# Kernel tuning notes

Hardware: AMD Instinct MI355X
Metric: run time of the kernel (lower is better)

The kernel has to match this reference:

```python
import jax, jax.numpy as jnp
import numpy as np

B, N, IN_DIM, HID, OUT, E = 2, 50000, 64, 256, 128, 500000

def setup_inputs() -> dict:
    key = jax.random.key(0)
    ks = jax.random.split(key, 8)
    s = lambda fan_in: 1.0 / np.sqrt(fan_in)
    x = jax.random.normal(ks[0], (B, N, IN_DIM), dtype=jnp.float32)
    edges = jax.random.randint(ks[1], (E, 2), 0, N, dtype=jnp.int64)
    return {
        "x": x,
        "edges": edges,
        "ew1": jax.random.normal(ks[2], (2 * IN_DIM, HID), dtype=jnp.float32) * s(2 * IN_DIM),
        "eb1": jnp.zeros((HID,), jnp.float32),
        "ew2": jax.random.normal(ks[3], (HID, OUT), dtype=jnp.float32) * s(HID),
        "eb2": jnp.zeros((OUT,), jnp.float32),
        "nw1": jax.random.normal(ks[4], (IN_DIM, HID), dtype=jnp.float32) * s(IN_DIM),
        "nb1": jnp.zeros((HID,), jnp.float32),
        "nw2": jax.random.normal(ks[5], (HID, OUT), dtype=jnp.float32) * s(HID),
        "nb2": jnp.zeros((OUT,), jnp.float32),
        "dw": jax.random.normal(ks[6], (OUT, IN_DIM), dtype=jnp.float32) * s(OUT),
        "db": jnp.zeros((IN_DIM,), jnp.float32),
    }

def _mlp(z, w1, b1, w2, b2):
    return jax.nn.relu(z @ w1 + b1) @ w2 + b2

def reference(x, edges, ew1, eb1, ew2, eb2, nw1, nb1, nw2, nb2, dw, db):
    u, v = edges[:, 0], edges[:, 1]
    # node embedding: [B, N, OUT]
    h = _mlp(x, nw1, nb1, nw2, nb2)
    # per-edge MLP on concatenated endpoint features: [B, E, OUT]
    edge_input = jnp.concatenate([x[:, u], x[:, v]], axis=-1)  # [B, E, 2*IN]
    edge_emb = _mlp(edge_input, ew1, eb1, ew2, eb2)
    # scatter-add edge message to both endpoints
    messages = jnp.zeros_like(h).at[:, u].add(edge_emb).at[:, v].add(edge_emb)
    h = h + messages
    recon = h @ dw + db  # [B, N, IN]
    return recon
```

## Files before the change

kernel.cpp:

```cpp
#include <hip/hip_runtime.h>
#include <hip/hip_bf16.h>

#define BB   2
#define NN   50000
#define BN   100000
#define NE   500000
#define NSB  196

#define EPITCH 136
#define XPITCH 72
#define HPITCH 264
#define RPITCH 72

using u16 = unsigned short;
using u32 = unsigned int;
typedef __attribute__((ext_vector_type(8))) short short8;
typedef __attribute__((ext_vector_type(4))) short short4v;
typedef __attribute__((ext_vector_type(4))) float f32x4;

__device__ __forceinline__ u16 f2bf(float f) {
    union { float f; u32 u; } w; w.f = f;
    return (u16)((w.u + 0x7fffu + ((w.u >> 16) & 1u)) >> 16);
}

__global__ __launch_bounds__(256) void csr_zero(int* __restrict__ cursor) {
    int i = blockIdx.x * 256 + threadIdx.x;
    if (i < NN) cursor[i] = 0;
}

__global__ __launch_bounds__(256) void csr_hist(const int* __restrict__ edges,
                                                int* __restrict__ cursor) {
    int e = blockIdx.x * 256 + threadIdx.x;
    if (e < NE) {
        atomicAdd(&cursor[edges[2*e]], 1);
        atomicAdd(&cursor[edges[2*e+1]], 1);
    }
}

__global__ __launch_bounds__(256) void scan_pass1(const int* __restrict__ cursor,
                                                  int* __restrict__ bsum) {
    __shared__ int s[256];
    const int t = threadIdx.x;
    int i = blockIdx.x * 256 + t;
    s[t] = (i < NN) ? cursor[i] : 0;
    __syncthreads();
    for (int d = 128; d > 0; d >>= 1) {
        if (t < d) s[t] += s[t + d];
        __syncthreads();
    }
    if (t == 0) bsum[blockIdx.x] = s[0];
}

__global__ __launch_bounds__(256) void scan_pass2(const int* __restrict__ bsum,
                                                  int* __restrict__ boff) {
    __shared__ int s[256];
    const int t = threadIdx.x;
    s[t] = (t < NSB) ? bsum[t] : 0;
    __syncthreads();
    for (int d = 1; d < 256; d <<= 1) {
        int v = (t >= d) ? s[t - d] : 0;
        __syncthreads();
        s[t] += v;
        __syncthreads();
    }
    if (t <= NSB) boff[t] = (t == 0) ? 0 : s[t - 1];
}

__global__ __launch_bounds__(256) void scan_pass3(int* __restrict__ cursor,
                                                  const int* __restrict__ boff,
                                                  int* __restrict__ off) {
    __shared__ int s[256];
    const int t = threadIdx.x;
    int i = blockIdx.x * 256 + t;
    int v = (i < NN) ? cursor[i] : 0;
    s[t] = v;
    __syncthreads();
    for (int d = 1; d < 256; d <<= 1) {
        int p = (t >= d) ? s[t - d] : 0;
        __syncthreads();
        s[t] += p;
        __syncthreads();
    }
    int excl = boff[blockIdx.x] + s[t] - v;
    if (i < NN) { off[i] = excl; cursor[i] = excl; }
    if (i == NN - 1) off[NN] = excl + v;
}

__global__ __launch_bounds__(256) void csr_fill(const int* __restrict__ edges,
                                                int* __restrict__ cursor,
                                                int* __restrict__ pos) {
    int e = blockIdx.x * 256 + threadIdx.x;
    if (e < NE) {
        pos[2*e]     = atomicAdd(&cursor[edges[2*e]], 1);
        pos[2*e + 1] = atomicAdd(&cursor[edges[2*e+1]], 1);
    }
}

__global__ __launch_bounds__(256) void swizzle_w1(
    const float* __restrict__ ew1, const float* __restrict__ nw1,
    u16* __restrict__ frag)
{
    int idx = blockIdx.x * 256 + threadIdx.x;
    if (idx >= 49152) return;
    const float* src; int KB, local;
    if (idx < 32768) { local = idx;         src = ew1; KB = 4; }
    else             { local = idx - 32768; src = nw1; KB = 2; }
    int j = local & 7, l = (local >> 3) & 63, rest = local >> 9;
    int kblk = rest % KB, ntile = rest / KB;
    int n = ntile * 16 + (l & 15);
    int k = kblk * 32 + ((l >> 4) << 3) + j;
    frag[idx] = f2bf(src[k * 256 + n]);
}

__global__ __launch_bounds__(256) void fuse_w2(
    const float* __restrict__ ew2, const float* __restrict__ nw2,
    const float* __restrict__ dw, u16* __restrict__ frag)
{
    int idx = blockIdx.x * 256 + threadIdx.x;
    if (idx >= 32768) return;
    const float* src = (idx < 16384) ? ew2 : nw2;
    int local = idx & 16383;
    int j = local & 7, l = (local >> 3) & 63, rest = local >> 9;
    int kblk = rest & 7, ntile = rest >> 3;
    int n = ntile * 16 + (l & 15);
    int k = kblk * 32 + ((l >> 4) << 3) + j;
    float s = 0.f;
    for (int jj = 0; jj < 128; ++jj) s = fmaf(src[k * 128 + jj], dw[jj * 64 + n], s);
    frag[49152 + idx] = f2bf(s);
}

__global__ __launch_bounds__(64) void fuse_bias(
    const float* __restrict__ eb2, const float* __restrict__ nb2,
    const float* __restrict__ dw, const float* __restrict__ db,
    float* __restrict__ bias2)
{
    int d = threadIdx.x;
    float se = 0.f, sn = 0.f;
    for (int j = 0; j < 128; ++j) {
        float w = dw[j * 64 + d];
        se = fmaf(eb2[j], w, se);
        sn = fmaf(nb2[j], w, sn);
    }
    bias2[d] = se;
    bias2[64 + d] = sn + db[d];
}

__global__ __launch_bounds__(256) void x_to_bf16(const float* __restrict__ x,
                                                 u16* __restrict__ xbf)
{
    int i = blockIdx.x * 256 + threadIdx.x;
    if (i >= BN * 16) return;
    float4 g = ((const float4*)x)[i];
    short4v s;
    s.x = (short)f2bf(g.x); s.y = (short)f2bf(g.y);
    s.z = (short)f2bf(g.z); s.w = (short)f2bf(g.w);
    *(short4v*)(xbf + (size_t)i * 4) = s;
}

__global__ __launch_bounds__(256) void node_mlp_kernel(
    const u16* __restrict__ xbf, const float* __restrict__ nb1,
    const float* __restrict__ bias2, const u16* __restrict__ frag,
    float* __restrict__ out)
{
    __shared__ u16 xs[64 * XPITCH];
    __shared__ u16 hid[64 * HPITCH];
    const int t = threadIdx.x;
    const int wave = t >> 6, l = t & 63, lane15 = l & 15, quad = l >> 4;
    const int r0 = blockIdx.x * 64;
    const int valid = min(64, BN - r0);

    #pragma unroll
    for (int it = 0; it < 2; ++it) {
        int i = t + it * 256;
        int m = i >> 3, c8 = i & 7;
        int row = min(r0 + m, BN - 1);
        uint4 q = ((const uint4*)xbf)[(size_t)row * 8 + c8];
        *(uint4*)(xs + m * XPITCH + c8 * 8) = q;
    }
    __syncthreads();

    {
        f32x4 acc[4][4];
        #pragma unroll
        for (int i = 0; i < 4; ++i)
            #pragma unroll
            for (int mt = 0; mt < 4; ++mt) acc[i][mt] = f32x4{0.f,0.f,0.f,0.f};
        const u16* w1 = frag + 32768;
        #pragma unroll
        for (int kblk = 0; kblk < 2; ++kblk) {
            short8 bf[4], af[4];
            #pragma unroll
            for (int mt = 0; mt < 4; ++mt)
                bf[mt] = *(const short8*)(xs + (mt*16 + lane15) * XPITCH + kblk*32 + quad*8);
            #pragma unroll
            for (int i = 0; i < 4; ++i)
                af[i] = *(const short8*)(w1 + (((wave*4 + i)*2 + kblk)*64 + l) * 8);
            #pragma unroll
            for (int i = 0; i < 4; ++i)
                #pragma unroll
                for (int mt = 0; mt < 4; ++mt)
                    acc[i][mt] = __builtin_amdgcn_mfma_f32_16x16x32_bf16(af[i], bf[mt], acc[i][mt], 0, 0, 0);
        }
        #pragma unroll
        for (int i = 0; i < 4; ++i) {
            int n0 = (wave*4 + i)*16 + quad*4;
            float4 bv = *(const float4*)(nb1 + n0);
            #pragma unroll
            for (int mt = 0; mt < 4; ++mt) {
                int m = mt*16 + lane15;
                short4v s;
                s.x = (short)f2bf(fmaxf(acc[i][mt][0] + bv.x, 0.f));
                s.y = (short)f2bf(fmaxf(acc[i][mt][1] + bv.y, 0.f));
                s.z = (short)f2bf(fmaxf(acc[i][mt][2] + bv.z, 0.f));
                s.w = (short)f2bf(fmaxf(acc[i][mt][3] + bv.w, 0.f));
                *(short4v*)(hid + m * HPITCH + n0) = s;
            }
        }
    }
    __syncthreads();

    {
        f32x4 acc[4];
        #pragma unroll
        for (int mt = 0; mt < 4; ++mt) acc[mt] = f32x4{0.f,0.f,0.f,0.f};
        const u16* w2 = frag + 65536;
        #pragma unroll
        for (int kblk = 0; kblk < 8; ++kblk) {
            short8 bf[4], af;
            #pragma unroll
            for (int mt = 0; mt < 4; ++mt)
                bf[mt] = *(const short8*)(hid + (mt*16 + lane15) * HPITCH + kblk*32 + quad*8);
            af = *(const short8*)(w2 + ((wave*8 + kblk)*64 + l) * 8);
            #pragma unroll
            for (int mt = 0; mt < 4; ++mt)
                acc[mt] = __builtin_amdgcn_mfma_f32_16x16x32_bf16(af, bf[mt], acc[mt], 0, 0, 0);
        }
        int n0 = wave*16 + quad*4;
        float4 bv = *(const float4*)(bias2 + 64 + n0);
        #pragma unroll
        for (int mt = 0; mt < 4; ++mt) {
            int m = mt*16 + lane15;
            if (m < valid) {
                float4 o;
                o.x = acc[mt][0] + bv.x; o.y = acc[mt][1] + bv.y;
                o.z = acc[mt][2] + bv.z; o.w = acc[mt][3] + bv.w;
                *(float4*)(out + (size_t)(r0 + m) * 64 + n0) = o;
            }
        }
    }
}

__global__ __launch_bounds__(256) void edge_emb_kernel(
    const u16* __restrict__ xbf, const int* __restrict__ edges,
    const float* __restrict__ eb1, const float* __restrict__ bias2,
    const u16* __restrict__ frag, const int* __restrict__ pos,
    u16* __restrict__ perm, int b)
{
    __shared__ u16 ein[64 * EPITCH];
    __shared__ u16 hid[64 * HPITCH];
    __shared__ int us[64], vs[64], ps[64], qs[64];
    const int t = threadIdx.x;
    const int wave = t >> 6, l = t & 63, lane15 = l & 15, quad = l >> 4;
    const int e0 = blockIdx.x * 64;
    const int valid = min(64, NE - e0);

    if (t < 64) {
        int e = min(e0 + t, NE - 1);
        us[t] = edges[2 * e];
        vs[t] = edges[2 * e + 1];
        ps[t] = pos[2 * e];
        qs[t] = pos[2 * e + 1];
    }
    __syncthreads();

    #pragma unroll
    for (int it = 0; it < 4; ++it) {
        int i = t + it * 256;
        int m = i >> 4, c = i & 15;
        int half = c >> 3, c8 = c & 7;
        int node = half ? vs[m] : us[m];
        uint4 q = ((const uint4*)xbf)[(size_t)(b * NN + node) * 8 + c8];
        *(uint4*)(ein + m * EPITCH + half * 64 + c8 * 8) = q;
    }
    __syncthreads();

    {
        f32x4 acc[4][4];
        #pragma unroll
        for (int i = 0; i < 4; ++i)
            #pragma unroll
            for (int mt = 0; mt < 4; ++mt) acc[i][mt] = f32x4{0.f,0.f,0.f,0.f};
        const u16* w1 = frag;
        #pragma unroll
        for (int kblk = 0; kblk < 4; ++kblk) {
            short8 bf[4], af[4];
            #pragma unroll
            for (int mt = 0; mt < 4; ++mt)
                bf[mt] = *(const short8*)(ein + (mt*16 + lane15) * EPITCH + kblk*32 + quad*8);
            #pragma unroll
            for (int i = 0; i < 4; ++i)
                af[i] = *(const short8*)(w1 + (((wave*4 + i)*4 + kblk)*64 + l) * 8);
            #pragma unroll
            for (int i = 0; i < 4; ++i)
                #pragma unroll
                for (int mt = 0; mt < 4; ++mt)
                    acc[i][mt] = __builtin_amdgcn_mfma_f32_16x16x32_bf16(af[i], bf[mt], acc[i][mt], 0, 0, 0);
        }
        #pragma unroll
        for (int i = 0; i < 4; ++i) {
            int n0 = (wave*4 + i)*16 + quad*4;
            float4 bv = *(const float4*)(eb1 + n0);
            #pragma unroll
            for (int mt = 0; mt < 4; ++mt) {
                int m = mt*16 + lane15;
                short4v s;
                s.x = (short)f2bf(fmaxf(acc[i][mt][0] + bv.x, 0.f));
                s.y = (short)f2bf(fmaxf(acc[i][mt][1] + bv.y, 0.f));
                s.z = (short)f2bf(fmaxf(acc[i][mt][2] + bv.z, 0.f));
                s.w = (short)f2bf(fmaxf(acc[i][mt][3] + bv.w, 0.f));
                *(short4v*)(hid + m * HPITCH + n0) = s;
            }
        }
    }
    __syncthreads();

    {
        f32x4 acc[4];
        #pragma unroll
        for (int mt = 0; mt < 4; ++mt) acc[mt] = f32x4{0.f,0.f,0.f,0.f};
        const u16* w2 = frag + 49152;
        #pragma unroll
        for (int kblk = 0; kblk < 8; ++kblk) {
            short8 bf[4], af;
            #pragma unroll
            for (int mt = 0; mt < 4; ++mt)
                bf[mt] = *(const short8*)(hid + (mt*16 + lane15) * HPITCH + kblk*32 + quad*8);
            af = *(const short8*)(w2 + ((wave*8 + kblk)*64 + l) * 8);
            #pragma unroll
            for (int mt = 0; mt < 4; ++mt)
                acc[mt] = __builtin_amdgcn_mfma_f32_16x16x32_bf16(af, bf[mt], acc[mt], 0, 0, 0);
        }
        int n0 = wave*16 + quad*4;
        float4 bv = *(const float4*)(bias2 + n0);
        #pragma unroll
        for (int mt = 0; mt < 4; ++mt) {
            int m = mt*16 + lane15;
            short4v s;
            s.x = (short)f2bf(acc[mt][0] + bv.x);
            s.y = (short)f2bf(acc[mt][1] + bv.y);
            s.z = (short)f2bf(acc[mt][2] + bv.z);
            s.w = (short)f2bf(acc[mt][3] + bv.w);
            *(short4v*)(ein + m * RPITCH + n0) = s;
        }
    }
    __syncthreads();

    #pragma unroll
    for (int it = 0; it < 4; ++it) {
        int i = t + it * 256;
        int dest = i >> 3, c8 = i & 7;
        int m = dest >> 1;
        if (m < valid) {
            int p = (dest & 1) ? qs[m] : ps[m];
            ((uint4*)(perm + (size_t)p * 64))[c8] = *(const uint4*)(ein + m * RPITCH + c8 * 8);
        }
    }
}

__global__ __launch_bounds__(256) void gather_kernel(
    const u32* __restrict__ perm32, const int* __restrict__ off,
    float* __restrict__ out, int b)
{
    const int t = threadIdx.x, wave = t >> 6, l = t & 63;
    const int n = blockIdx.x * 4 + wave;
    const int base = off[n], cnt = off[n + 1] - base;
    if (cnt == 0) return;
    const int slot = l >> 4, c8h = l & 15;
    float a0 = 0.f, a1 = 0.f, a2 = 0.f, a3 = 0.f;
    for (int j0 = 0; j0 < cnt; j0 += 4) {
        int j = j0 + slot;
        size_t r = (size_t)(base + min(j, cnt - 1));
        const u32* rp = perm32 + r * 32 + 2 * c8h;
        u32 w0 = rp[0], w1 = rp[1];
        if (j < cnt) {
            union { u32 u; float f; } x0, x1, x2, x3;
            x0.u = w0 << 16; x1.u = w0 & 0xffff0000u;
            x2.u = w1 << 16; x3.u = w1 & 0xffff0000u;
            a0 += x0.f; a1 += x1.f; a2 += x2.f; a3 += x3.f;
        }
    }
    a0 += __shfl_xor(a0, 16); a1 += __shfl_xor(a1, 16);
    a2 += __shfl_xor(a2, 16); a3 += __shfl_xor(a3, 16);
    a0 += __shfl_xor(a0, 32); a1 += __shfl_xor(a1, 32);
    a2 += __shfl_xor(a2, 32); a3 += __shfl_xor(a3, 32);
    if (l < 16) {
        float4* p = (float4*)(out + (size_t)(b * NN + n) * 64 + 4 * l);
        float4 h = *p;
        h.x += a0; h.y += a1; h.z += a2; h.w += a3;
        *p = h;
    }
}

extern "C" void kernel_launch(void* const* d_in, const int* in_sizes, int n_in,
                              void* d_out, int out_size, void* d_ws, size_t ws_size,
                              hipStream_t stream) {
    const float* x     = (const float*)d_in[0];
    const int*   edges = (const int*)d_in[1];
    const float* ew1   = (const float*)d_in[2];
    const float* eb1   = (const float*)d_in[3];
    const float* ew2   = (const float*)d_in[4];
    const float* eb2   = (const float*)d_in[5];
    const float* nw1   = (const float*)d_in[6];
    const float* nb1   = (const float*)d_in[7];
    const float* nw2   = (const float*)d_in[8];
    const float* nb2   = (const float*)d_in[9];
    const float* dw    = (const float*)d_in[10];
    const float* db    = (const float*)d_in[11];
    float* out = (float*)d_out;

    char* w = (char*)d_ws;
    size_t o = 0;
    auto take = [&](size_t bytes) { char* p = w + o; o = (o + bytes + 511) & ~(size_t)511; return p; };
    u16*   frag   = (u16*)  take(81920 * 2);
    float* bias2  = (float*)take(128 * 4);
    int*   cursor = (int*)  take((size_t)NN * 4);
    int*   off    = (int*)  take((size_t)(NN + 1) * 4);
    int*   bsum   = (int*)  take((size_t)(NSB + 1) * 4);
    int*   boff   = (int*)  take((size_t)(NSB + 1) * 4);
    int*   pos    = (int*)  take((size_t)2 * NE * 4);
    u16*   xbf    = (u16*)  take((size_t)BN * 64 * 2);
    u16*   perm   = (u16*)  take((size_t)2 * NE * 64 * 2);

    csr_zero<<<NSB, 256, 0, stream>>>(cursor);
    csr_hist<<<(NE + 255) / 256, 256, 0, stream>>>(edges, cursor);
    scan_pass1<<<NSB, 256, 0, stream>>>(cursor, bsum);
    scan_pass2<<<1, 256, 0, stream>>>(bsum, boff);
    scan_pass3<<<NSB, 256, 0, stream>>>(cursor, boff, off);
    csr_fill<<<(NE + 255) / 256, 256, 0, stream>>>(edges, cursor, pos);

    swizzle_w1<<<192, 256, 0, stream>>>(ew1, nw1, frag);
    fuse_w2<<<128, 256, 0, stream>>>(ew2, nw2, dw, frag);
    fuse_bias<<<1, 64, 0, stream>>>(eb2, nb2, dw, db, bias2);
    x_to_bf16<<<(BN * 16 + 255) / 256, 256, 0, stream>>>(x, xbf);

    node_mlp_kernel<<<(BN + 63) / 64, 256, 0, stream>>>(xbf, nb1, bias2, frag, out);

    for (int b = 0; b < BB; ++b) {
        edge_emb_kernel<<<(NE + 63) / 64, 256, 0, stream>>>(xbf, edges, eb1, bias2, frag, pos, perm, b);
        gather_kernel<<<NN / 4, 256, 0, stream>>>((const u32*)perm, off, out, b);
    }
}
```

Measured before the change: 465.4 us.

## Fuse x bf16 conversion into node MLP, use packed cvt, unroll gather

Removes the separate x_to_bf16 kernel: node_mlp_kernel now reads fp32 x, converts it to bf16 into shared memory, and also writes the bf16 copy used later by the edge kernel. All bf16 conversions switch to a packed hardware convert builtin when the compiler provides one. The gather loop handles two edge rows per lane per iteration to raise memory-level parallelism. fuse_bias is split across 128 threads. The aim is to cut one launch and one extra pass over x, plus ALU work in the epilogues, at the cost of slightly more global stores from the node kernel and possible rounding differences from the builtin convert.

```diff
diff --git a/kernel.cpp b/kernel.cpp
--- a/kernel.cpp
+++ b/kernel.cpp
@@ -21,6 +21,22 @@
 __device__ __forceinline__ u16 f2bf(float f) {
     union { float f; u32 u; } w; w.f = f;
     return (u16)((w.u + 0x7fffu + ((w.u >> 16) & 1u)) >> 16);
+}
+
+#if defined(__has_builtin)
+#if __has_builtin(__builtin_amdgcn_cvt_pk_bf16_f32)
+#define HAVE_CVTPK 1
+#endif
+#endif
+
+__device__ __forceinline__ u32 pack_bf(float lo, float hi) {
+#ifdef HAVE_CVTPK
+    auto r = __builtin_amdgcn_cvt_pk_bf16_f32(lo, hi);
+    u32 out; __builtin_memcpy(&out, &r, sizeof(out));
+    return out;
+#else
+    return ((u32)f2bf(hi) << 16) | (u32)f2bf(lo);
+#endif
 }
 
 __global__ __launch_bounds__(256) void csr_zero(int* __restrict__ cursor) {
@@ -129,38 +145,25 @@
     frag[49152 + idx] = f2bf(s);
 }
 
-__global__ __launch_bounds__(64) void fuse_bias(
+__global__ __launch_bounds__(128) void fuse_bias(
     const float* __restrict__ eb2, const float* __restrict__ nb2,
     const float* __restrict__ dw, const float* __restrict__ db,
     float* __restrict__ bias2)
 {
-    int d = threadIdx.x;
-    float se = 0.f, sn = 0.f;
-    for (int j = 0; j < 128; ++j) {
-        float w = dw[j * 64 + d];
-        se = fmaf(eb2[j], w, se);
-        sn = fmaf(nb2[j], w, sn);
-    }
-    bias2[d] = se;
-    bias2[64 + d] = sn + db[d];
-}
-
-__global__ __launch_bounds__(256) void x_to_bf16(const float* __restrict__ x,
-                                                 u16* __restrict__ xbf)
-{
-    int i = blockIdx.x * 256 + threadIdx.x;
-    if (i >= BN * 16) return;
-    float4 g = ((const float4*)x)[i];
-    short4v s;
-    s.x = (short)f2bf(g.x); s.y = (short)f2bf(g.y);
-    s.z = (short)f2bf(g.z); s.w = (short)f2bf(g.w);
-    *(short4v*)(xbf + (size_t)i * 4) = s;
+    int t = threadIdx.x;
+    int d = t & 63;
+    const float* bsrc = (t >= 64) ? nb2 : eb2;
+    float s = 0.f;
+    #pragma unroll 4
+    for (int j = 0; j < 128; ++j) s = fmaf(bsrc[j], dw[j * 64 + d], s);
+    if (t >= 64) bias2[64 + d] = s + db[d];
+    else         bias2[d] = s;
 }
 
 __global__ __launch_bounds__(256) void node_mlp_kernel(
-    const u16* __restrict__ xbf, const float* __restrict__ nb1,
+    const float* __restrict__ x, const float* __restrict__ nb1,
     const float* __restrict__ bias2, const u16* __restrict__ frag,
-    float* __restrict__ out)
+    u16* __restrict__ xbf, float* __restrict__ out)
 {
     __shared__ u16 xs[64 * XPITCH];
     __shared__ u16 hid[64 * HPITCH];
@@ -170,12 +173,14 @@
     const int valid = min(64, BN - r0);
 
     #pragma unroll
-    for (int it = 0; it < 2; ++it) {
+    for (int it = 0; it < 4; ++it) {
         int i = t + it * 256;
-        int m = i >> 3, c8 = i & 7;
+        int m = i >> 4, c4 = i & 15;
         int row = min(r0 + m, BN - 1);
-        uint4 q = ((const uint4*)xbf)[(size_t)row * 8 + c8];
-        *(uint4*)(xs + m * XPITCH + c8 * 8) = q;
+        float4 g = ((const float4*)x)[(size_t)row * 16 + c4];
+        uint2 q = make_uint2(pack_bf(g.x, g.y), pack_bf(g.z, g.w));
+        *(uint2*)(xs + m * XPITCH + c4 * 4) = q;
+        *(uint2*)(xbf + (size_t)row * 64 + c4 * 4) = q;
     }
     __syncthreads();
 
@@ -208,12 +213,10 @@
             #pragma unroll
             for (int mt = 0; mt < 4; ++mt) {
                 int m = mt*16 + lane15;
-                short4v s;
-                s.x = (short)f2bf(fmaxf(acc[i][mt][0] + bv.x, 0.f));
-                s.y = (short)f2bf(fmaxf(acc[i][mt][1] + bv.y, 0.f));
-                s.z = (short)f2bf(fmaxf(acc[i][mt][2] + bv.z, 0.f));
-                s.w = (short)f2bf(fmaxf(acc[i][mt][3] + bv.w, 0.f));
-                *(short4v*)(hid + m * HPITCH + n0) = s;
+                uint2 q = make_uint2(
+                    pack_bf(fmaxf(acc[i][mt][0] + bv.x, 0.f), fmaxf(acc[i][mt][1] + bv.y, 0.f)),
+                    pack_bf(fmaxf(acc[i][mt][2] + bv.z, 0.f), fmaxf(acc[i][mt][3] + bv.w, 0.f)));
+                *(uint2*)(hid + m * HPITCH + n0) = q;
             }
         }
     }
@@ -313,12 +316,10 @@
             #pragma unroll
             for (int mt = 0; mt < 4; ++mt) {
                 int m = mt*16 + lane15;
-                short4v s;
-                s.x = (short)f2bf(fmaxf(acc[i][mt][0] + bv.x, 0.f));
-                s.y = (short)f2bf(fmaxf(acc[i][mt][1] + bv.y, 0.f));
-                s.z = (short)f2bf(fmaxf(acc[i][mt][2] + bv.z, 0.f));
-                s.w = (short)f2bf(fmaxf(acc[i][mt][3] + bv.w, 0.f));
-                *(short4v*)(hid + m * HPITCH + n0) = s;
+                uint2 q = make_uint2(
+                    pack_bf(fmaxf(acc[i][mt][0] + bv.x, 0.f), fmaxf(acc[i][mt][1] + bv.y, 0.f)),
+                    pack_bf(fmaxf(acc[i][mt][2] + bv.z, 0.f), fmaxf(acc[i][mt][3] + bv.w, 0.f)));
+                *(uint2*)(hid + m * HPITCH + n0) = q;
             }
         }
     }
@@ -345,12 +346,10 @@
         #pragma unroll
         for (int mt = 0; mt < 4; ++mt) {
             int m = mt*16 + lane15;
-            short4v s;
-            s.x = (short)f2bf(acc[mt][0] + bv.x);
-            s.y = (short)f2bf(acc[mt][1] + bv.y);
-            s.z = (short)f2bf(acc[mt][2] + bv.z);
-            s.w = (short)f2bf(acc[mt][3] + bv.w);
-            *(short4v*)(ein + m * RPITCH + n0) = s;
+            uint2 q = make_uint2(
+                pack_bf(acc[mt][0] + bv.x, acc[mt][1] + bv.y),
+                pack_bf(acc[mt][2] + bv.z, acc[mt][3] + bv.w));
+            *(uint2*)(ein + m * RPITCH + n0) = q;
         }
     }
     __syncthreads();
@@ -377,15 +376,21 @@
     if (cnt == 0) return;
     const int slot = l >> 4, c8h = l & 15;
     float a0 = 0.f, a1 = 0.f, a2 = 0.f, a3 = 0.f;
-    for (int j0 = 0; j0 < cnt; j0 += 4) {
-        int j = j0 + slot;
-        size_t r = (size_t)(base + min(j, cnt - 1));
-        const u32* rp = perm32 + r * 32 + 2 * c8h;
-        u32 w0 = rp[0], w1 = rp[1];
-        if (j < cnt) {
-            union { u32 u; float f; } x0, x1, x2, x3;
-            x0.u = w0 << 16; x1.u = w0 & 0xffff0000u;
-            x2.u = w1 << 16; x3.u = w1 & 0xffff0000u;
+    for (int j0 = 0; j0 < cnt; j0 += 8) {
+        int jA = j0 + slot, jB = j0 + 4 + slot;
+        const u32* rpA = perm32 + (size_t)(base + min(jA, cnt - 1)) * 32 + 2 * c8h;
+        const u32* rpB = perm32 + (size_t)(base + min(jB, cnt - 1)) * 32 + 2 * c8h;
+        u32 wA0 = rpA[0], wA1 = rpA[1];
+        u32 wB0 = rpB[0], wB1 = rpB[1];
+        union { u32 u; float f; } x0, x1, x2, x3;
+        if (jA < cnt) {
+            x0.u = wA0 << 16; x1.u = wA0 & 0xffff0000u;
+            x2.u = wA1 << 16; x3.u = wA1 & 0xffff0000u;
+            a0 += x0.f; a1 += x1.f; a2 += x2.f; a3 += x3.f;
+        }
+        if (jB < cnt) {
+            x0.u = wB0 << 16; x1.u = wB0 & 0xffff0000u;
+            x2.u = wB1 << 16; x3.u = wB1 & 0xffff0000u;
             a0 += x0.f; a1 += x1.f; a2 += x2.f; a3 += x3.f;
         }
     }
@@ -440,10 +445,9 @@
 
     swizzle_w1<<<192, 256, 0, stream>>>(ew1, nw1, frag);
     fuse_w2<<<128, 256, 0, stream>>>(ew2, nw2, dw, frag);
-    fuse_bias<<<1, 64, 0, stream>>>(eb2, nb2, dw, db, bias2);
-    x_to_bf16<<<(BN * 16 + 255) / 256, 256, 0, stream>>>(x, xbf);
-
-    node_mlp_kernel<<<(BN + 63) / 64, 256, 0, stream>>>(xbf, nb1, bias2, frag, out);
+    fuse_bias<<<1, 128, 0, stream>>>(eb2, nb2, dw, db, bias2);
+
+    node_mlp_kernel<<<(BN + 63) / 64, 256, 0, stream>>>(x, nb1, bias2, frag, xbf, out);
 
     for (int b = 0; b < BB; ++b) {
         edge_emb_kernel<<<(NE + 63) / 64, 256, 0, stream>>>(xbf, edges, eb1, bias2, frag, pos, perm, b);
```

New measurement: 452.9 us. -2.7%, faster.
